# Kernel tuning notes

Hardware: AMD Instinct MI355X
Metric: run time of the kernel (lower is better)

## Reference

```python
import jax, jax.numpy as jnp
import numpy as np

B, T, D, H = 4, 2048, 1024, 16
DK = D // H


def setup_inputs() -> dict:
    key = jax.random.key(0)
    ks = jax.random.split(key, 13)
    s = 1.0 / np.sqrt(D)
    inp = {
        "query": jax.random.normal(ks[0], (B, T, D), jnp.float32),
        "key": jax.random.normal(ks[1], (B, T, D), jnp.float32),
        "value": jax.random.normal(ks[2], (B, T, D), jnp.float32),
        "mask": jax.random.randint(ks[3], (B, 1, T), 0, 2) > 0,
        "wq": jax.random.normal(ks[4], (D, D), jnp.float32) * s,
        "bq": jnp.zeros((D,), jnp.float32),
        "wk": jax.random.normal(ks[5], (D, D), jnp.float32) * s,
        "bk": jnp.zeros((D,), jnp.float32),
        "wv": jax.random.normal(ks[6], (D, D), jnp.float32) * s,
        "bv": jnp.zeros((D,), jnp.float32),
        "wo": jax.random.normal(ks[7], (D, D), jnp.float32) * s,
        "bo": jnp.zeros((D,), jnp.float32),
    }
    return inp


def reference(query, key, value, mask, wq, bq, wk, bk, wv, bv, wo, bo):
    b = query.shape[0]
    # QKV projections -> [b, h, t, d_k]
    q = (query @ wq.T + bq).reshape(b, -1, H, DK).transpose(0, 2, 1, 3)
    k = (key @ wk.T + bk).reshape(b, -1, H, DK).transpose(0, 2, 1, 3)
    v = (value @ wv.T + bv).reshape(b, -1, H, DK).transpose(0, 2, 1, 3)
    # scaled dot-product scores [b, h, tq, tk]
    scores = jnp.einsum("bhqd,bhkd->bhqk", q, k) / jnp.sqrt(jnp.float32(DK))
    m = mask[:, None, :, :]  # [b, 1, 1, tk] broadcast over heads/queries
    scores = jnp.where(m, -10000.0, scores)
    attn = jax.nn.softmax(scores, axis=-1)
    attn = jnp.where(m, 0.0, attn)
    x = jnp.einsum("bhqk,bhkd->bhqd", attn, v)
    x = x.transpose(0, 2, 1, 3).reshape(b, -1, H * DK)
    return x @ wo.T + bo
```

## Files before the change

### kernel.cpp

```cpp
#include <hip/hip_runtime.h>

#define B_ 4
#define T_ 2048
#define D_ 1024
#define H_ 16
#define DK_ 64
#define M_ (B_*T_)

typedef __attribute__((ext_vector_type(4))) float f32x4;
typedef __attribute__((ext_vector_type(8))) short s16x8;
typedef unsigned short u16t;
typedef unsigned int   u32t;
typedef unsigned long long u64t;

__device__ __forceinline__ u16t f2bf(float x){
  u32t u = __float_as_uint(x);
  return (u16t)((u + 0x7FFFu + ((u >> 16) & 1u)) >> 16);
}

__device__ __forceinline__ f32x4 mfma16(s16x8 a, s16x8 b, f32x4 c){
  return __builtin_amdgcn_mfma_f32_16x16x32_bf16(a, b, c, 0, 0, 0);
}

__device__ __forceinline__ void gload16(const void* g, void* l){
  __builtin_amdgcn_global_load_lds(
      (const __attribute__((address_space(1))) u32t*)g,
      (__attribute__((address_space(3))) u32t*)l, 16, 0, 0);
}

__global__ __launch_bounds__(256) void cvt_bf16(const float* __restrict__ src,
                                                u16t* __restrict__ dst, int n4){
  int i = blockIdx.x * 256 + threadIdx.x;
  if (i < n4){
    float4 v = ((const float4*)src)[i];
    u64t o = (u64t)f2bf(v.x) | ((u64t)f2bf(v.y) << 16)
           | ((u64t)f2bf(v.z) << 32) | ((u64t)f2bf(v.w) << 48);
    ((u64t*)dst)[i] = o;
  }
}

#define BM 128
#define BN 128
#define BKG 32

template<typename OT>
__global__ __launch_bounds__(256, 2) void gemm_bt(const u16t* __restrict__ A,
                                                  const u16t* __restrict__ Bw,
                                                  const float* __restrict__ bias,
                                                  OT* __restrict__ C,
                                                  int Mi, int Ni, int Ki){
  __shared__ u16t As[BM * BKG];
  __shared__ u16t Bs[BN * BKG];
  const int tid = threadIdx.x, lane = tid & 63, w = tid >> 6;
  const int wm = w >> 1, wn = w & 1;
  const int bm = blockIdx.x * BM, bn = blockIdx.y * BN;

  f32x4 acc[4][4];
  const f32x4 z4 = {0.f, 0.f, 0.f, 0.f};
  #pragma unroll
  for (int i = 0; i < 4; i++)
    #pragma unroll
    for (int j = 0; j < 4; j++) acc[i][j] = z4;

  for (int kk = 0; kk < Ki; kk += BKG){
    #pragma unroll
    for (int i = 0; i < 2; i++){
      int y   = (w * 2 + i) * 1024 + lane * 16;
      int row = y >> 6;
      int ke  = (y >> 4) & 3;
      gload16(A  + (size_t)(bm + row) * Ki + kk + ke * 8, (char*)As + (w * 2 + i) * 1024);
      gload16(Bw + (size_t)(bn + row) * Ki + kk + ke * 8, (char*)Bs + (w * 2 + i) * 1024);
    }
    __syncthreads();
    s16x8 af[4], bf[4];
    #pragma unroll
    for (int i = 0; i < 4; i++){
      af[i] = *(const s16x8*)(As + (size_t)(wm * 64 + i * 16 + (lane & 15)) * BKG + (lane >> 4) * 8);
      bf[i] = *(const s16x8*)(Bs + (size_t)(wn * 64 + i * 16 + (lane & 15)) * BKG + (lane >> 4) * 8);
    }
    #pragma unroll
    for (int i = 0; i < 4; i++)
      #pragma unroll
      for (int j = 0; j < 4; j++)
        acc[i][j] = mfma16(af[i], bf[j], acc[i][j]);
    __syncthreads();
  }

  #pragma unroll
  for (int j = 0; j < 4; j++){
    int n = bn + wn * 64 + j * 16 + (lane & 15);
    float bv = bias[n];
    #pragma unroll
    for (int i = 0; i < 4; i++){
      int m0 = bm + wm * 64 + i * 16 + (lane >> 4) * 4;
      #pragma unroll
      for (int r = 0; r < 4; r++){
        float v = acc[i][j][r] + bv;
        if constexpr (sizeof(OT) == 4)
          C[(size_t)(m0 + r) * Ni + n] = v;
        else
          C[(size_t)(m0 + r) * Ni + n] = f2bf(v);
      }
    }
  }
}

__global__ __launch_bounds__(256) void transpose_v(const u16t* __restrict__ V,
                                                   u16t* __restrict__ Vt){
  __shared__ u16t tle[64][65];
  const int bh = blockIdx.y, b = bh >> 4, h = bh & 15;
  const int t0 = blockIdx.x * 64;
  const u16t* vp = V + (size_t)(b * T_ + t0) * D_ + h * DK_;
  #pragma unroll
  for (int i = 0; i < 16; i++){
    int idx = threadIdx.x + i * 256;
    int tr = idx >> 6, dk = idx & 63;
    tle[tr][dk] = vp[(size_t)tr * D_ + dk];
  }
  __syncthreads();
  u16t* op = Vt + (size_t)bh * DK_ * T_ + t0;
  #pragma unroll
  for (int i = 0; i < 16; i++){
    int idx = threadIdx.x + i * 256;
    int dk = idx >> 6, tr = idx & 63;
    op[(size_t)dk * T_ + tr] = tle[tr][dk];
  }
}

#define KVB 64

__global__ __launch_bounds__(512) void attn(const u16t* __restrict__ Q,
                                            const u16t* __restrict__ K,
                                            const u16t* __restrict__ Vt,
                                            const int* __restrict__ mask,
                                            u16t* __restrict__ X){
  __shared__ u16t Ks[2][KVB * 64];
  __shared__ u16t Vs[2][KVB * 64];

  const int tid = threadIdx.x;
  const int lane = tid & 63;
  const int w = tid >> 6;
  const int q16 = lane & 15, g = lane >> 4;
  const int bh = blockIdx.y, b = bh >> 4, h = bh & 15;
  const int tq = blockIdx.x * 128 + w * 16 + q16;

  const u16t* qp = Q + (size_t)(b * T_ + tq) * D_ + h * DK_ + g * 8;
  s16x8 qf0 = *(const s16x8*)(qp);
  s16x8 qf1 = *(const s16x8*)(qp + 32);

  const f32x4 z4 = {0.f, 0.f, 0.f, 0.f};
  f32x4 acc[4];
  #pragma unroll
  for (int d = 0; d < 4; d++) acc[d] = z4;
  float mrun = -1e30f, lsum = 0.f;

  const u16t* kbase = K + (size_t)b * T_ * D_ + h * DK_;
  const u16t* vbase = Vt + (size_t)bh * DK_ * T_;
  const int* mb = mask + (size_t)b * T_;

  const int srow = tid >> 3;
  const int sc   = (tid & 7) ^ (srow & 7);
  const u16t* ksrc = kbase + (size_t)srow * D_ + sc * 8;
  const u16t* vsrc = vbase + (size_t)srow * T_ + sc * 8;

  gload16(ksrc, (u16t*)Ks[0] + w * 512);
  gload16(vsrc, (u16t*)Vs[0] + w * 512);
  __syncthreads();

  const int NT = T_ / KVB;
  for (int t = 0; t < NT; t++){
    const int buf = t & 1;
    if (t + 1 < NT){
      gload16(ksrc + (size_t)(t + 1) * KVB * D_, (u16t*)Ks[buf ^ 1] + w * 512);
      gload16(vsrc + (size_t)(t + 1) * KVB,      (u16t*)Vs[buf ^ 1] + w * 512);
    }
    const u16t* Kb = Ks[buf];
    const u16t* Vb = Vs[buf];

    #pragma unroll
    for (int s = 0; s < 2; s++){
      const int kt = t * KVB + s * 32;
      const int r0 = s * 32 + q16, r1 = r0 + 16;
      s16x8 k00 = *(const s16x8*)(Kb + r0 * 64 + (((g    ) ^ (r0 & 7)) << 3));
      s16x8 k01 = *(const s16x8*)(Kb + r0 * 64 + (((g + 4) ^ (r0 & 7)) << 3));
      s16x8 k10 = *(const s16x8*)(Kb + r1 * 64 + (((g    ) ^ (r1 & 7)) << 3));
      s16x8 k11 = *(const s16x8*)(Kb + r1 * 64 + (((g + 4) ^ (r1 & 7)) << 3));
      f32x4 s0 = z4, s1 = z4;
      s0 = mfma16(k00, qf0, s0); s0 = mfma16(k01, qf1, s0);
      s1 = mfma16(k10, qf0, s1); s1 = mfma16(k11, qf1, s1);

      int4 mm0 = *(const int4*)(mb + kt + g * 4);
      int4 mm1 = *(const int4*)(mb + kt + 16 + g * 4);
      int mA[4] = {mm0.x, mm0.y, mm0.z, mm0.w};
      int mBv[4] = {mm1.x, mm1.y, mm1.z, mm1.w};
      float sv0[4], sv1[4];
      #pragma unroll
      for (int r = 0; r < 4; r++){
        sv0[r] = mA[r]  ? -3e38f : s0[r] * 0.125f;
        sv1[r] = mBv[r] ? -3e38f : s1[r] * 0.125f;
      }
      float mx = sv0[0];
      #pragma unroll
      for (int r = 1; r < 4; r++) mx = fmaxf(mx, sv0[r]);
      #pragma unroll
      for (int r = 0; r < 4; r++) mx = fmaxf(mx, sv1[r]);
      mx = fmaxf(mx, __shfl_xor(mx, 16, 64));
      mx = fmaxf(mx, __shfl_xor(mx, 32, 64));
      float mnew = fmaxf(mrun, mx);
      float fsc = __expf(mrun - mnew);
      float p0[4], p1[4], ts = 0.f;
      #pragma unroll
      for (int r = 0; r < 4; r++){
        p0[r] = __expf(sv0[r] - mnew);
        p1[r] = __expf(sv1[r] - mnew);
        ts += p0[r] + p1[r];
      }
      ts += __shfl_xor(ts, 16, 64);
      ts += __shfl_xor(ts, 32, 64);
      lsum = lsum * fsc + ts;
      mrun = mnew;
      #pragma unroll
      for (int d = 0; d < 4; d++) acc[d] = acc[d] * fsc;

      u32t w0a = ((u32t)f2bf(p0[1]) << 16) | f2bf(p0[0]);
      u32t w1a = ((u32t)f2bf(p0[3]) << 16) | f2bf(p0[2]);
      u32t w0b = ((u32t)f2bf(p1[1]) << 16) | f2bf(p1[0]);
      u32t w1b = ((u32t)f2bf(p1[3]) << 16) | f2bf(p1[2]);
      int laneA = ((g & 1) << 5) | q16;
      u32t a0 = (u32t)__shfl((int)w0a, laneA, 64);
      u32t a1 = (u32t)__shfl((int)w1a, laneA, 64);
      u32t a2 = (u32t)__shfl((int)w0b, laneA, 64);
      u32t a3 = (u32t)__shfl((int)w1b, laneA, 64);
      u32t b0 = (u32t)__shfl((int)w0a, laneA + 16, 64);
      u32t b1 = (u32t)__shfl((int)w1a, laneA + 16, 64);
      u32t b2 = (u32t)__shfl((int)w0b, laneA + 16, 64);
      u32t b3 = (u32t)__shfl((int)w1b, laneA + 16, 64);
      bool hi = (g >= 2);
      union { u32t u[4]; s16x8 v; } pf;
      pf.u[0] = hi ? a2 : a0;
      pf.u[1] = hi ? a3 : a1;
      pf.u[2] = hi ? b2 : b0;
      pf.u[3] = hi ? b3 : b1;

      #pragma unroll
      for (int d = 0; d < 4; d++){
        const int vr = d * 16 + q16;
        s16x8 vf = *(const s16x8*)(Vb + vr * 64 + (((s * 4 + g) ^ (vr & 7)) << 3));
        acc[d] = mfma16(vf, pf.v, acc[d]);
      }
    }
    __syncthreads();
  }

  float inv = (lsum > 0.f) ? 1.0f / lsum : 0.f;
  u16t* xp = X + (size_t)(b * T_ + tq) * D_ + h * DK_ + g * 4;
  #pragma unroll
  for (int d = 0; d < 4; d++){
    u32t o0 = ((u32t)f2bf(acc[d][1] * inv) << 16) | f2bf(acc[d][0] * inv);
    u32t o1 = ((u32t)f2bf(acc[d][3] * inv) << 16) | f2bf(acc[d][2] * inv);
    *(u64t*)(xp + d * 16) = ((u64t)o1 << 32) | o0;
  }
}

extern "C" void kernel_launch(void* const* d_in, const int* in_sizes, int n_in,
                              void* d_out, int out_size, void* d_ws, size_t ws_size,
                              hipStream_t stream){
  (void)in_sizes; (void)n_in; (void)out_size; (void)ws_size;
  const float* query = (const float*)d_in[0];
  const float* key   = (const float*)d_in[1];
  const float* value = (const float*)d_in[2];
  const int*   mask  = (const int*)d_in[3];
  const float* wq = (const float*)d_in[4];
  const float* bq = (const float*)d_in[5];
  const float* wk = (const float*)d_in[6];
  const float* bk = (const float*)d_in[7];
  const float* wv = (const float*)d_in[8];
  const float* bv = (const float*)d_in[9];
  const float* wo = (const float*)d_in[10];
  const float* bo = (const float*)d_in[11];

  const size_t A = (size_t)M_ * D_;
  const size_t W = (size_t)D_ * D_;
  u16t* ws  = (u16t*)d_ws;
  u16t* qb  = ws;
  u16t* kb  = ws + A;
  u16t* vb  = ws + 2 * A;
  u16t* Qm  = ws + 3 * A;
  u16t* Km  = ws + 4 * A;
  u16t* Vm  = ws + 5 * A;
  u16t* wqb = ws + 6 * A;
  u16t* wkb = wqb + W;
  u16t* wvb = wqb + 2 * W;
  u16t* wob = wqb + 3 * W;
  u16t* Vt  = qb;
  u16t* Xm  = kb;

  int nA4 = (int)(A / 4), nW4 = (int)(W / 4);
  cvt_bf16<<<nA4 / 256, 256, 0, stream>>>(query, qb, nA4);
  cvt_bf16<<<nA4 / 256, 256, 0, stream>>>(key,   kb, nA4);
  cvt_bf16<<<nA4 / 256, 256, 0, stream>>>(value, vb, nA4);
  cvt_bf16<<<nW4 / 256, 256, 0, stream>>>(wq, wqb, nW4);
  cvt_bf16<<<nW4 / 256, 256, 0, stream>>>(wk, wkb, nW4);
  cvt_bf16<<<nW4 / 256, 256, 0, stream>>>(wv, wvb, nW4);
  cvt_bf16<<<nW4 / 256, 256, 0, stream>>>(wo, wob, nW4);

  dim3 gg(M_ / BM, D_ / BN);
  gemm_bt<u16t><<<gg, 256, 0, stream>>>(qb, wqb, bq, Qm, M_, D_, D_);
  gemm_bt<u16t><<<gg, 256, 0, stream>>>(kb, wkb, bk, Km, M_, D_, D_);
  gemm_bt<u16t><<<gg, 256, 0, stream>>>(vb, wvb, bv, Vm, M_, D_, D_);

  transpose_v<<<dim3(T_ / 64, B_ * H_), 256, 0, stream>>>(Vm, Vt);

  attn<<<dim3(T_ / 128, B_ * H_), 512, 0, stream>>>(Qm, Km, Vt, mask, Xm);

  gemm_bt<float><<<gg, 256, 0, stream>>>(Xm, wob, bo, (float*)d_out, M_, D_, D_);
}
```

Baseline: 457.9 us.

## Batch conversion and QKV GEMM launches, add lazy softmax rescale and packed bf16 cvt

Merges the seven conversion launches into two kernels and the three QKV projection GEMMs into one launch over a z grid dimension. The int mask becomes a precomputed additive float bias, so masking turns into an fma. The online softmax now rescales the accumulator only when the running max grows by more than 8, and the P probabilities are packed with the hardware v_cvt_pk_bf16_f32 instruction. This reduces launch overhead and per-tile ALU work in the attention loop, at the cost of probabilities that may exceed 1 before normalization, with some risk to bf16 precision.

```diff
diff --git a/kernel.cpp b/kernel.cpp
--- a/kernel.cpp
+++ b/kernel.cpp
@@ -18,6 +18,12 @@
   return (u16t)((u + 0x7FFFu + ((u >> 16) & 1u)) >> 16);
 }
 
+__device__ __forceinline__ u32t cvt_pk_bf16(float lo, float hi){
+  u32t r;
+  asm("v_cvt_pk_bf16_f32 %0, %1, %2" : "=v"(r) : "v"(lo), "v"(hi));
+  return r;
+}
+
 __device__ __forceinline__ f32x4 mfma16(s16x8 a, s16x8 b, f32x4 c){
   return __builtin_amdgcn_mfma_f32_16x16x32_bf16(a, b, c, 0, 0, 0);
 }
@@ -28,14 +34,44 @@
       (__attribute__((address_space(3))) u32t*)l, 16, 0, 0);
 }
 
-__global__ __launch_bounds__(256) void cvt_bf16(const float* __restrict__ src,
-                                                u16t* __restrict__ dst, int n4){
-  int i = blockIdx.x * 256 + threadIdx.x;
-  if (i < n4){
-    float4 v = ((const float4*)src)[i];
-    u64t o = (u64t)f2bf(v.x) | ((u64t)f2bf(v.y) << 16)
-           | ((u64t)f2bf(v.z) << 32) | ((u64t)f2bf(v.w) << 48);
-    ((u64t*)dst)[i] = o;
+__device__ __forceinline__ void cvt_body(const float* __restrict__ src,
+                                         u16t* __restrict__ dst, int i){
+  float4 v = ((const float4*)src)[i];
+  u64t o = (u64t)f2bf(v.x) | ((u64t)f2bf(v.y) << 16)
+         | ((u64t)f2bf(v.z) << 32) | ((u64t)f2bf(v.w) << 48);
+  ((u64t*)dst)[i] = o;
+}
+
+__global__ __launch_bounds__(256) void cvt_inputs(const float* __restrict__ q,
+                                                  const float* __restrict__ k,
+                                                  const float* __restrict__ v,
+                                                  u16t* __restrict__ dst){
+  int blk = blockIdx.x;
+  const float* src;
+  u16t* d;
+  const int SEG = (M_ * D_ / 4) / 256;
+  if (blk < SEG){ src = q; d = dst; }
+  else if (blk < 2*SEG){ src = k; d = dst + (size_t)M_*D_; blk -= SEG; }
+  else { src = v; d = dst + 2*(size_t)M_*D_; blk -= 2*SEG; }
+  cvt_body(src, d, blk * 256 + threadIdx.x);
+}
+
+__global__ __launch_bounds__(256) void cvt_weights(const float* __restrict__ wq,
+                                                   const float* __restrict__ wk,
+                                                   const float* __restrict__ wv,
+                                                   const float* __restrict__ wo,
+                                                   u16t* __restrict__ wdst,
+                                                   const int* __restrict__ mask,
+                                                   float* __restrict__ maskf){
+  int blk = blockIdx.x;
+  const int SEG = (D_ * D_ / 4) / 256;
+  if (blk < 4*SEG){
+    const float* src = (blk < SEG) ? wq : (blk < 2*SEG) ? wk : (blk < 3*SEG) ? wv : wo;
+    u16t* d = wdst + (size_t)(blk / SEG) * D_ * D_;
+    cvt_body(src, d, (blk % SEG) * 256 + threadIdx.x);
+  } else {
+    int i = (blk - 4*SEG) * 256 + threadIdx.x;
+    maskf[i] = mask[i] ? -3e38f : 0.f;
   }
 }
 
@@ -44,13 +80,12 @@
 #define BKG 32
 
 template<typename OT>
-__global__ __launch_bounds__(256, 2) void gemm_bt(const u16t* __restrict__ A,
-                                                  const u16t* __restrict__ Bw,
-                                                  const float* __restrict__ bias,
-                                                  OT* __restrict__ C,
-                                                  int Mi, int Ni, int Ki){
-  __shared__ u16t As[BM * BKG];
-  __shared__ u16t Bs[BN * BKG];
+__device__ __forceinline__ void gemm_core(const u16t* __restrict__ A,
+                                          const u16t* __restrict__ Bw,
+                                          const float* __restrict__ bias,
+                                          OT* __restrict__ C,
+                                          int Ni, int Ki,
+                                          u16t* As, u16t* Bs){
   const int tid = threadIdx.x, lane = tid & 63, w = tid >> 6;
   const int wm = w >> 1, wn = w & 1;
   const int bm = blockIdx.x * BM, bn = blockIdx.y * BN;
@@ -105,6 +140,29 @@
   }
 }
 
+__global__ __launch_bounds__(256, 2) void gemm_qkv(const u16t* __restrict__ in0,
+                                                   const u16t* __restrict__ w0,
+                                                   const float* __restrict__ b0,
+                                                   const float* __restrict__ b1,
+                                                   const float* __restrict__ b2,
+                                                   u16t* __restrict__ out0){
+  __shared__ u16t As[BM * BKG];
+  __shared__ u16t Bs[BN * BKG];
+  const int z = blockIdx.z;
+  const float* bias = (z == 0) ? b0 : (z == 1) ? b1 : b2;
+  gemm_core<u16t>(in0 + (size_t)z * M_ * D_, w0 + (size_t)z * D_ * D_, bias,
+                  out0 + (size_t)z * M_ * D_, D_, D_, As, Bs);
+}
+
+__global__ __launch_bounds__(256, 2) void gemm_out(const u16t* __restrict__ A,
+                                                   const u16t* __restrict__ Bw,
+                                                   const float* __restrict__ bias,
+                                                   float* __restrict__ C){
+  __shared__ u16t As[BM * BKG];
+  __shared__ u16t Bs[BN * BKG];
+  gemm_core<float>(A, Bw, bias, C, D_, D_, As, Bs);
+}
+
 __global__ __launch_bounds__(256) void transpose_v(const u16t* __restrict__ V,
                                                    u16t* __restrict__ Vt){
   __shared__ u16t tle[64][65];
@@ -132,7 +190,7 @@
 __global__ __launch_bounds__(512) void attn(const u16t* __restrict__ Q,
                                             const u16t* __restrict__ K,
                                             const u16t* __restrict__ Vt,
-                                            const int* __restrict__ mask,
+                                            const float* __restrict__ maskf,
                                             u16t* __restrict__ X){
   __shared__ u16t Ks[2][KVB * 64];
   __shared__ u16t Vs[2][KVB * 64];
@@ -156,7 +214,7 @@
 
   const u16t* kbase = K + (size_t)b * T_ * D_ + h * DK_;
   const u16t* vbase = Vt + (size_t)bh * DK_ * T_;
-  const int* mb = mask + (size_t)b * T_;
+  const float* mb = maskf + (size_t)b * T_;
 
   const int srow = tid >> 3;
   const int sc   = (tid & 7) ^ (srow & 7);
@@ -189,43 +247,47 @@
       s0 = mfma16(k00, qf0, s0); s0 = mfma16(k01, qf1, s0);
       s1 = mfma16(k10, qf0, s1); s1 = mfma16(k11, qf1, s1);
 
-      int4 mm0 = *(const int4*)(mb + kt + g * 4);
-      int4 mm1 = *(const int4*)(mb + kt + 16 + g * 4);
-      int mA[4] = {mm0.x, mm0.y, mm0.z, mm0.w};
-      int mBv[4] = {mm1.x, mm1.y, mm1.z, mm1.w};
+      float4 mb0 = *(const float4*)(mb + kt + g * 4);
+      float4 mb1 = *(const float4*)(mb + kt + 16 + g * 4);
+      float bA[4] = {mb0.x, mb0.y, mb0.z, mb0.w};
+      float bB[4] = {mb1.x, mb1.y, mb1.z, mb1.w};
       float sv0[4], sv1[4];
       #pragma unroll
       for (int r = 0; r < 4; r++){
-        sv0[r] = mA[r]  ? -3e38f : s0[r] * 0.125f;
-        sv1[r] = mBv[r] ? -3e38f : s1[r] * 0.125f;
-      }
-      float mx = sv0[0];
-      #pragma unroll
-      for (int r = 1; r < 4; r++) mx = fmaxf(mx, sv0[r]);
-      #pragma unroll
-      for (int r = 0; r < 4; r++) mx = fmaxf(mx, sv1[r]);
+        sv0[r] = fmaf(s0[r], 0.125f, bA[r]);
+        sv1[r] = fmaf(s1[r], 0.125f, bB[r]);
+      }
+      float mx = fmaxf(sv0[0], sv0[1]);
+      mx = fmaxf(mx, fmaxf(sv0[2], sv0[3]));
+      mx = fmaxf(mx, fmaxf(sv1[0], sv1[1]));
+      mx = fmaxf(mx, fmaxf(sv1[2], sv1[3]));
       mx = fmaxf(mx, __shfl_xor(mx, 16, 64));
       mx = fmaxf(mx, __shfl_xor(mx, 32, 64));
-      float mnew = fmaxf(mrun, mx);
-      float fsc = __expf(mrun - mnew);
+
+      if (__any(mx > mrun + 8.0f)){
+        float mnew = fmaxf(mrun, mx);
+        float fsc = __expf(mrun - mnew);
+        lsum *= fsc;
+        #pragma unroll
+        for (int d = 0; d < 4; d++) acc[d] = acc[d] * fsc;
+        mrun = mnew;
+      }
+
       float p0[4], p1[4], ts = 0.f;
       #pragma unroll
       for (int r = 0; r < 4; r++){
-        p0[r] = __expf(sv0[r] - mnew);
-        p1[r] = __expf(sv1[r] - mnew);
+        p0[r] = __expf(sv0[r] - mrun);
+        p1[r] = __expf(sv1[r] - mrun);
         ts += p0[r] + p1[r];
       }
       ts += __shfl_xor(ts, 16, 64);
       ts += __shfl_xor(ts, 32, 64);
-      lsum = lsum * fsc + ts;
-      mrun = mnew;
-      #pragma unroll
-      for (int d = 0; d < 4; d++) acc[d] = acc[d] * fsc;
-
-      u32t w0a = ((u32t)f2bf(p0[1]) << 16) | f2bf(p0[0]);
-      u32t w1a = ((u32t)f2bf(p0[3]) << 16) | f2bf(p0[2]);
-      u32t w0b = ((u32t)f2bf(p1[1]) << 16) | f2bf(p1[0]);
-      u32t w1b = ((u32t)f2bf(p1[3]) << 16) | f2bf(p1[2]);
+      lsum += ts;
+
+      u32t w0a = cvt_pk_bf16(p0[0], p0[1]);
+      u32t w1a = cvt_pk_bf16(p0[2], p0[3]);
+      u32t w0b = cvt_pk_bf16(p1[0], p1[1]);
+      u32t w1b = cvt_pk_bf16(p1[2], p1[3]);
       int laneA = ((g & 1) << 5) | q16;
       u32t a0 = (u32t)__shfl((int)w0a, laneA, 64);
       u32t a1 = (u32t)__shfl((int)w1a, laneA, 64);
@@ -283,35 +345,25 @@
   const size_t W = (size_t)D_ * D_;
   u16t* ws  = (u16t*)d_ws;
   u16t* qb  = ws;
-  u16t* kb  = ws + A;
-  u16t* vb  = ws + 2 * A;
   u16t* Qm  = ws + 3 * A;
   u16t* Km  = ws + 4 * A;
   u16t* Vm  = ws + 5 * A;
   u16t* wqb = ws + 6 * A;
-  u16t* wkb = wqb + W;
-  u16t* wvb = wqb + 2 * W;
   u16t* wob = wqb + 3 * W;
+  float* maskf = (float*)(wqb + 4 * W);
   u16t* Vt  = qb;
-  u16t* Xm  = kb;
-
-  int nA4 = (int)(A / 4), nW4 = (int)(W / 4);
-  cvt_bf16<<<nA4 / 256, 256, 0, stream>>>(query, qb, nA4);
-  cvt_bf16<<<nA4 / 256, 256, 0, stream>>>(key,   kb, nA4);
-  cvt_bf16<<<nA4 / 256, 256, 0, stream>>>(value, vb, nA4);
-  cvt_bf16<<<nW4 / 256, 256, 0, stream>>>(wq, wqb, nW4);
-  cvt_bf16<<<nW4 / 256, 256, 0, stream>>>(wk, wkb, nW4);
-  cvt_bf16<<<nW4 / 256, 256, 0, stream>>>(wv, wvb, nW4);
-  cvt_bf16<<<nW4 / 256, 256, 0, stream>>>(wo, wob, nW4);
-
-  dim3 gg(M_ / BM, D_ / BN);
-  gemm_bt<u16t><<<gg, 256, 0, stream>>>(qb, wqb, bq, Qm, M_, D_, D_);
-  gemm_bt<u16t><<<gg, 256, 0, stream>>>(kb, wkb, bk, Km, M_, D_, D_);
-  gemm_bt<u16t><<<gg, 256, 0, stream>>>(vb, wvb, bv, Vm, M_, D_, D_);
+  u16t* Xm  = qb + A;
+
+  const int SEGA = (int)(A / 4) / 256;
+  const int SEGW = (int)(W / 4) / 256;
+  cvt_inputs<<<3 * SEGA, 256, 0, stream>>>(query, key, value, qb);
+  cvt_weights<<<4 * SEGW + 32, 256, 0, stream>>>(wq, wk, wv, wo, wqb, mask, maskf);
+
+  gemm_qkv<<<dim3(M_ / BM, D_ / BN, 3), 256, 0, stream>>>(qb, wqb, bq, bk, bv, Qm);
 
   transpose_v<<<dim3(T_ / 64, B_ * H_), 256, 0, stream>>>(Vm, Vt);
 
-  attn<<<dim3(T_ / 128, B_ * H_), 512, 0, stream>>>(Qm, Km, Vt, mask, Xm);
-
-  gemm_bt<float><<<gg, 256, 0, stream>>>(Xm, wob, bo, (float*)d_out, M_, D_, D_);
-}
+  attn<<<dim3(T_ / 128, B_ * H_), 512, 0, stream>>>(Qm, Km, Vt, maskf, Xm);
+
+  gemm_out<<<dim3(M_ / BM, D_ / BN), 256, 0, stream>>>(Xm, wob, bo, (float*)d_out);
+}
```

New measurement: 421.3 us. 1.09x faster.
